# Performance work log

Hardware: AMD Instinct MI355X
Metric: run time of the kernel (lower is better)

Reference implementation:

```python
import jax, jax.numpy as jnp
import numpy as np

TEMPERATURE = 1.0
EPS = 1e-12


def _l2_normalize(x, axis):
    # torch F.normalize: x / max(||x||_2, eps)
    n = jnp.sqrt(jnp.sum(x * x, axis=axis, keepdims=True))
    return x / jnp.maximum(n, EPS)


def setup_inputs() -> dict:
    key = jax.random.key(0)
    k1, k2 = jax.random.split(key)
    B, C, H, W = 2, 128, 128, 256
    K = 20
    features = jax.random.normal(k1, (B, C, H, W), dtype=jnp.float32)
    prototypes = jax.random.normal(k2, (K, C), dtype=jnp.float32)
    distance_scale = jnp.ones((1,), dtype=jnp.float32)
    return {"features": features, "prototypes": prototypes, "distance_scale": distance_scale}


def reference(features, prototypes, distance_scale):
    # features: [B, C, H, W] -> transpose(1,3) -> [B, W, H, C]
    f = jnp.transpose(features, (0, 3, 2, 1))
    # torch F.normalize default dim=1: on [B, W, H, C] this is the W axis (faithful)
    fn = _l2_normalize(f, axis=1)
    # prototypes [K, C], normalized along dim=1 (features)
    pn = _l2_normalize(prototypes, axis=1)
    # exact euclidean cdist (donot_use_mm): broadcasted diff [B, W, H, K, C]
    diff = fn[:, :, :, None, :] - pn[None, None, None, :, :]
    dist = jnp.sqrt(jnp.sum(diff * diff, axis=-1))  # [B, W, H, K]
    dist = jnp.abs(distance_scale) * dist
    # transpose(3,1): [B, K, H, W]
    logits = -jnp.transpose(dist, (0, 3, 2, 1))
    return logits / TEMPERATURE
```

## Files before the change

kernel.cpp:

```cpp
#include <hip/hip_runtime.h>
#include <math.h>

#define B 2
#define C 128
#define H 128
#define W 256
#define K 20
#define HW (H * W)
#define SO_STRIDE 260

typedef float f32x4 __attribute__((ext_vector_type(4)));
typedef short bf16x8 __attribute__((ext_vector_type(8)));

__device__ __forceinline__ unsigned f2bf_bits(float x) {
    unsigned u = __float_as_uint(x);
    return (u + 0x7FFFu + ((u >> 16) & 1u)) >> 16;
}
__device__ __forceinline__ float bf_to_f(unsigned bits) {
    return __uint_as_float(bits << 16);
}

__global__ __launch_bounds__(1024) void isomax_fused(
    const float* __restrict__ feats, const float* __restrict__ protos,
    const float* __restrict__ dscale, float* __restrict__ out)
{
    __shared__ float s_rn[C];
    __shared__ float s_rp[32];
    __shared__ float s_pp[32];
    __shared__ float s_S[W];
    __shared__ __align__(16) float s_o[K * SO_STRIDE];

    const int tid  = threadIdx.x;
    const int wave = tid >> 6, lane = tid & 63;
    const int quad = lane >> 4, l16 = lane & 15;
    const int bh   = blockIdx.x;
    const int b    = bh >> 7, h = bh & 127;
    const int m0   = wave * 16;

    #pragma unroll
    for (int rd = 0; rd < 2; ++rd) {
        const int k = rd * 16 + wave;
        if (k < K) {
            const float* p = protos + k * C;
            const float a = p[lane], b2 = p[lane + 64];
            float ss = fmaf(a, a, b2 * b2);
            #pragma unroll
            for (int off = 32; off > 0; off >>= 1) ss += __shfl_xor(ss, off, 64);
            const float rp = 1.0f / fmaxf(sqrtf(ss), 1e-12f);
            const float q0 = bf_to_f(f2bf_bits(a * rp));
            const float q1 = bf_to_f(f2bf_bits(b2 * rp));
            float s2 = fmaf(q0, q0, q1 * q1);
            #pragma unroll
            for (int off = 32; off > 0; off >>= 1) s2 += __shfl_xor(s2, off, 64);
            if (lane == 0) { s_rp[k] = rp; s_pp[k] = s2; }
        }
    }

    for (int c = wave; c < C; c += 16) {
        const float* row = feats + ((size_t)((b * C + c) * H + h)) * W;
        const float4 v = ((const float4*)row)[lane];
        float ss = fmaf(v.x, v.x, fmaf(v.y, v.y, fmaf(v.z, v.z, v.w * v.w)));
        #pragma unroll
        for (int off = 32; off > 0; off >>= 1) ss += __shfl_xor(ss, off, 64);
        if (lane == 0) s_rn[c] = 1.0f / fmaxf(sqrtf(ss), 1e-12f);
    }
    __syncthreads();

    bf16x8 bfrag[4][2];
    #pragma unroll
    for (int t = 0; t < 2; ++t) {
        const int k = t * 16 + l16;
        const float rp = (k < K) ? s_rp[k] : 0.0f;
        #pragma unroll
        for (int ch = 0; ch < 4; ++ch) {
            bf16x8 f = {0, 0, 0, 0, 0, 0, 0, 0};
            if (k < K) {
                const float* pr = protos + k * C + ch * 32 + quad * 8;
                const float4 pa = *(const float4*)(pr);
                const float4 pb = *(const float4*)(pr + 4);
                f[0] = (short)f2bf_bits(pa.x * rp);
                f[1] = (short)f2bf_bits(pa.y * rp);
                f[2] = (short)f2bf_bits(pa.z * rp);
                f[3] = (short)f2bf_bits(pa.w * rp);
                f[4] = (short)f2bf_bits(pb.x * rp);
                f[5] = (short)f2bf_bits(pb.y * rp);
                f[6] = (short)f2bf_bits(pb.z * rp);
                f[7] = (short)f2bf_bits(pb.w * rp);
            }
            bfrag[ch][t] = f;
        }
    }

    f32x4 acc0 = {0.f, 0.f, 0.f, 0.f}, acc1 = {0.f, 0.f, 0.f, 0.f};
    float Sp = 0.f;
    const float* fbase = feats + ((size_t)(b * C) * H + h) * W + m0 + l16;
    #pragma unroll
    for (int ch = 0; ch < 4; ++ch) {
        bf16x8 af;
        #pragma unroll
        for (int j = 0; j < 8; ++j) {
            const int c = ch * 32 + quad * 8 + j;
            const float uf = fbase[(size_t)c * HW] * s_rn[c];
            const unsigned bits = f2bf_bits(uf);
            af[j] = (short)bits;
            const float ur = bf_to_f(bits);
            Sp = fmaf(ur, ur, Sp);
        }
        acc0 = __builtin_amdgcn_mfma_f32_16x16x32_bf16(af, bfrag[ch][0], acc0, 0, 0, 0);
        acc1 = __builtin_amdgcn_mfma_f32_16x16x32_bf16(af, bfrag[ch][1], acc1, 0, 0, 0);
    }

    Sp += __shfl_xor(Sp, 16, 64);
    Sp += __shfl_xor(Sp, 32, 64);
    if (lane < 16) s_S[m0 + lane] = Sp;
    __syncthreads();

    const float scale = fabsf(dscale[0]);
    const float pcol0 = s_pp[l16];
    const float pcol1 = (l16 < 4) ? s_pp[16 + l16] : 0.0f;
    #pragma unroll
    for (int r = 0; r < 4; ++r) {
        const int wl = m0 + quad * 4 + r;
        const float Sm = s_S[wl];
        const float d20 = fmaxf(Sm + pcol0 - 2.0f * acc0[r], 0.f);
        s_o[l16 * SO_STRIDE + wl] = -scale * sqrtf(d20);
        if (l16 < 4) {
            const float d21 = fmaxf(Sm + pcol1 - 2.0f * acc1[r], 0.f);
            s_o[(16 + l16) * SO_STRIDE + wl] = -scale * sqrtf(d21);
        }
    }
    __syncthreads();

    for (int i = tid; i < K * (W / 4); i += 1024) {
        const int k = i >> 6, g = i & 63;
        const float4 v = *(const float4*)&s_o[k * SO_STRIDE + g * 4];
        *(float4*)(out + ((size_t)(b * K + k)) * HW + h * W + g * 4) = v;
    }
}

extern "C" void kernel_launch(void* const* d_in, const int* in_sizes, int n_in,
                              void* d_out, int out_size, void* d_ws, size_t ws_size,
                              hipStream_t stream) {
    const float* feats  = (const float*)d_in[0];
    const float* protos = (const float*)d_in[1];
    const float* dscale = (const float*)d_in[2];
    float* out = (float*)d_out;

    isomax_fused<<<B * H, 1024, 0, stream>>>(feats, protos, dscale, out);
}
```

Before: 86.82 us.

## Stage normalized bf16 features in swizzled LDS instead of re-reading global

Each block now loads every feature row once with coalesced float4 loads, normalizes and packs it to bf16, and writes it into a 32 KB XOR-swizzled LDS tile, processing the channels in two passes. MFMA A-fragments are then read from LDS instead of through a second strided scalar pass over global memory. This removes the duplicate global read of the features and the uncoalesced per-channel loads. In exchange it adds extra barriers and a large LDS footprint that may limit blocks per CU.

```diff
diff --git a/kernel.cpp b/kernel.cpp
--- a/kernel.cpp
+++ b/kernel.cpp
@@ -24,7 +24,7 @@
     const float* __restrict__ feats, const float* __restrict__ protos,
     const float* __restrict__ dscale, float* __restrict__ out)
 {
-    __shared__ float s_rn[C];
+    __shared__ __align__(16) unsigned s_u32[64 * 128];
     __shared__ float s_rp[32];
     __shared__ float s_pp[32];
     __shared__ float s_S[W];
@@ -56,58 +56,74 @@
         }
     }
 
-    for (int c = wave; c < C; c += 16) {
-        const float* row = feats + ((size_t)((b * C + c) * H + h)) * W;
-        const float4 v = ((const float4*)row)[lane];
-        float ss = fmaf(v.x, v.x, fmaf(v.y, v.y, fmaf(v.z, v.z, v.w * v.w)));
-        #pragma unroll
-        for (int off = 32; off > 0; off >>= 1) ss += __shfl_xor(ss, off, 64);
-        if (lane == 0) s_rn[c] = 1.0f / fmaxf(sqrtf(ss), 1e-12f);
-    }
-    __syncthreads();
-
-    bf16x8 bfrag[4][2];
-    #pragma unroll
-    for (int t = 0; t < 2; ++t) {
-        const int k = t * 16 + l16;
-        const float rp = (k < K) ? s_rp[k] : 0.0f;
-        #pragma unroll
-        for (int ch = 0; ch < 4; ++ch) {
-            bf16x8 f = {0, 0, 0, 0, 0, 0, 0, 0};
-            if (k < K) {
-                const float* pr = protos + k * C + ch * 32 + quad * 8;
-                const float4 pa = *(const float4*)(pr);
-                const float4 pb = *(const float4*)(pr + 4);
-                f[0] = (short)f2bf_bits(pa.x * rp);
-                f[1] = (short)f2bf_bits(pa.y * rp);
-                f[2] = (short)f2bf_bits(pa.z * rp);
-                f[3] = (short)f2bf_bits(pa.w * rp);
-                f[4] = (short)f2bf_bits(pb.x * rp);
-                f[5] = (short)f2bf_bits(pb.y * rp);
-                f[6] = (short)f2bf_bits(pb.z * rp);
-                f[7] = (short)f2bf_bits(pb.w * rp);
-            }
-            bfrag[ch][t] = f;
-        }
-    }
-
     f32x4 acc0 = {0.f, 0.f, 0.f, 0.f}, acc1 = {0.f, 0.f, 0.f, 0.f};
     float Sp = 0.f;
-    const float* fbase = feats + ((size_t)(b * C) * H + h) * W + m0 + l16;
+    bf16x8 bfrag[4][2];
+
     #pragma unroll
-    for (int ch = 0; ch < 4; ++ch) {
-        bf16x8 af;
+    for (int pass = 0; pass < 2; ++pass) {
         #pragma unroll
-        for (int j = 0; j < 8; ++j) {
-            const int c = ch * 32 + quad * 8 + j;
-            const float uf = fbase[(size_t)c * HW] * s_rn[c];
-            const unsigned bits = f2bf_bits(uf);
-            af[j] = (short)bits;
-            const float ur = bf_to_f(bits);
-            Sp = fmaf(ur, ur, Sp);
+        for (int r = 0; r < 4; ++r) {
+            const int cc = wave * 4 + r;
+            const int c  = pass * 64 + cc;
+            const float* row = feats + ((size_t)((b * C + c) * H + h)) * W;
+            const float4 f4 = ((const float4*)row)[lane];
+            float ss = fmaf(f4.x, f4.x, fmaf(f4.y, f4.y, fmaf(f4.z, f4.z, f4.w * f4.w)));
+            #pragma unroll
+            for (int off = 32; off > 0; off >>= 1) ss += __shfl_xor(ss, off, 64);
+            const float rn = 1.0f / fmaxf(sqrtf(ss), 1e-12f);
+            const unsigned lo = f2bf_bits(f4.x * rn) | (f2bf_bits(f4.y * rn) << 16);
+            const unsigned hi = f2bf_bits(f4.z * rn) | (f2bf_bits(f4.w * rn) << 16);
+            const int word = cc * 128 + ((lane * 2) ^ (((cc >> 3) & 3) << 3));
+            uint2 pk; pk.x = lo; pk.y = hi;
+            *(uint2*)&s_u32[word] = pk;
         }
-        acc0 = __builtin_amdgcn_mfma_f32_16x16x32_bf16(af, bfrag[ch][0], acc0, 0, 0, 0);
-        acc1 = __builtin_amdgcn_mfma_f32_16x16x32_bf16(af, bfrag[ch][1], acc1, 0, 0, 0);
+        __syncthreads();
+
+        if (pass == 0) {
+            #pragma unroll
+            for (int t = 0; t < 2; ++t) {
+                const int k = t * 16 + l16;
+                const float rp = (k < K) ? s_rp[k] : 0.0f;
+                #pragma unroll
+                for (int ch = 0; ch < 4; ++ch) {
+                    bf16x8 f = {0, 0, 0, 0, 0, 0, 0, 0};
+                    if (k < K) {
+                        const float* pr = protos + k * C + ch * 32 + quad * 8;
+                        const float4 pa = *(const float4*)(pr);
+                        const float4 pb = *(const float4*)(pr + 4);
+                        f[0] = (short)f2bf_bits(pa.x * rp);
+                        f[1] = (short)f2bf_bits(pa.y * rp);
+                        f[2] = (short)f2bf_bits(pa.z * rp);
+                        f[3] = (short)f2bf_bits(pa.w * rp);
+                        f[4] = (short)f2bf_bits(pb.x * rp);
+                        f[5] = (short)f2bf_bits(pb.y * rp);
+                        f[6] = (short)f2bf_bits(pb.z * rp);
+                        f[7] = (short)f2bf_bits(pb.w * rp);
+                    }
+                    bfrag[ch][t] = f;
+                }
+            }
+        }
+
+        const int wadrw = ((m0 + l16) >> 1) ^ (quad << 3);
+        const unsigned sel = (unsigned)(l16 & 1);
+        #pragma unroll
+        for (int ch2 = 0; ch2 < 2; ++ch2) {
+            bf16x8 af;
+            #pragma unroll
+            for (int j = 0; j < 8; ++j) {
+                const int rowi = ch2 * 32 + quad * 8 + j;
+                const unsigned v = s_u32[rowi * 128 + wadrw];
+                af[j] = (short)(sel ? (v >> 16) : v);
+                const float ur = __uint_as_float(sel ? (v & 0xffff0000u) : (v << 16));
+                Sp = fmaf(ur, ur, Sp);
+            }
+            const int ch = pass * 2 + ch2;
+            acc0 = __builtin_amdgcn_mfma_f32_16x16x32_bf16(af, bfrag[ch][0], acc0, 0, 0, 0);
+            acc1 = __builtin_amdgcn_mfma_f32_16x16x32_bf16(af, bfrag[ch][1], acc1, 0, 0, 0);
+        }
+        __syncthreads();
     }
 
     Sp += __shfl_xor(Sp, 16, 64);
```

New measurement: 86.88 us. No clear change (+0.1%).

## Stage normalized bf16 feature tile in LDS to avoid re-reading global features

Applied to the files above, without the earlier changes.

Each block now loads its feature slice from global memory once into registers, computes the per-channel norms, and writes the normalized bf16-packed values into a swizzled shared-memory tile. The MFMA A-fragments are then read from LDS instead of issuing a second strided global read per element. Prototype normalization is also restructured so each wave handles two prototypes in parallel. This removes the duplicate global traffic and scattered loads at the cost of 64KB of extra LDS per block and more register pressure.

```diff
diff --git a/kernel.cpp b/kernel.cpp
--- a/kernel.cpp
+++ b/kernel.cpp
@@ -24,7 +24,7 @@
     const float* __restrict__ feats, const float* __restrict__ protos,
     const float* __restrict__ dscale, float* __restrict__ out)
 {
-    __shared__ float s_rn[C];
+    __shared__ __align__(16) unsigned s_u32[C * 128];
     __shared__ float s_rp[32];
     __shared__ float s_pp[32];
     __shared__ float s_S[W];
@@ -37,33 +37,80 @@
     const int b    = bh >> 7, h = bh & 127;
     const int m0   = wave * 16;
 
+    const float* fb = feats + (size_t)b * C * HW + h * W;
+
+    const int cA = wave * 8;
+    float4 fA[4];
     #pragma unroll
-    for (int rd = 0; rd < 2; ++rd) {
-        const int k = rd * 16 + wave;
-        if (k < K) {
-            const float* p = protos + k * C;
-            const float a = p[lane], b2 = p[lane + 64];
-            float ss = fmaf(a, a, b2 * b2);
-            #pragma unroll
-            for (int off = 32; off > 0; off >>= 1) ss += __shfl_xor(ss, off, 64);
-            const float rp = 1.0f / fmaxf(sqrtf(ss), 1e-12f);
-            const float q0 = bf_to_f(f2bf_bits(a * rp));
-            const float q1 = bf_to_f(f2bf_bits(b2 * rp));
-            float s2 = fmaf(q0, q0, q1 * q1);
-            #pragma unroll
-            for (int off = 32; off > 0; off >>= 1) s2 += __shfl_xor(s2, off, 64);
-            if (lane == 0) { s_rp[k] = rp; s_pp[k] = s2; }
+    for (int r = 0; r < 4; ++r)
+        fA[r] = ((const float4*)(fb + (size_t)(cA + r) * HW))[lane];
+
+    const int k0 = wave;
+    const int k1 = 16 + (wave & 3);
+    const float pa0 = protos[k0 * C + lane], pb0 = protos[k0 * C + lane + 64];
+    const float pa1 = protos[k1 * C + lane], pb1 = protos[k1 * C + lane + 64];
+
+    const int cB = cA + 4;
+    float4 fB[4];
+    #pragma unroll
+    for (int r = 0; r < 4; ++r)
+        fB[r] = ((const float4*)(fb + (size_t)(cB + r) * HW))[lane];
+
+    {
+        float ss0 = fmaf(pa0, pa0, pb0 * pb0);
+        float ss1 = fmaf(pa1, pa1, pb1 * pb1);
+        #pragma unroll
+        for (int off = 32; off > 0; off >>= 1) {
+            ss0 += __shfl_xor(ss0, off, 64);
+            ss1 += __shfl_xor(ss1, off, 64);
+        }
+        const float rp0 = 1.0f / fmaxf(sqrtf(ss0), 1e-12f);
+        const float rp1 = 1.0f / fmaxf(sqrtf(ss1), 1e-12f);
+        const float q00 = bf_to_f(f2bf_bits(pa0 * rp0));
+        const float q01 = bf_to_f(f2bf_bits(pb0 * rp0));
+        const float q10 = bf_to_f(f2bf_bits(pa1 * rp1));
+        const float q11 = bf_to_f(f2bf_bits(pb1 * rp1));
+        float s20 = fmaf(q00, q00, q01 * q01);
+        float s21 = fmaf(q10, q10, q11 * q11);
+        #pragma unroll
+        for (int off = 32; off > 0; off >>= 1) {
+            s20 += __shfl_xor(s20, off, 64);
+            s21 += __shfl_xor(s21, off, 64);
+        }
+        if (lane == 0) {
+            s_rp[k0] = rp0; s_pp[k0] = s20;
+            if (wave < 4) { s_rp[k1] = rp1; s_pp[k1] = s21; }
         }
     }
 
-    for (int c = wave; c < C; c += 16) {
-        const float* row = feats + ((size_t)((b * C + c) * H + h)) * W;
-        const float4 v = ((const float4*)row)[lane];
-        float ss = fmaf(v.x, v.x, fmaf(v.y, v.y, fmaf(v.z, v.z, v.w * v.w)));
-        #pragma unroll
-        for (int off = 32; off > 0; off >>= 1) ss += __shfl_xor(ss, off, 64);
-        if (lane == 0) s_rn[c] = 1.0f / fmaxf(sqrtf(ss), 1e-12f);
+    #define PROC_GROUP(fR, c0)                                                     \
+    {                                                                              \
+        float ss[4];                                                               \
+        _Pragma("unroll")                                                          \
+        for (int r = 0; r < 4; ++r) {                                              \
+            const float4 v = fR[r];                                                \
+            ss[r] = fmaf(v.x, v.x, fmaf(v.y, v.y, fmaf(v.z, v.z, v.w * v.w)));     \
+        }                                                                          \
+        _Pragma("unroll")                                                          \
+        for (int off = 32; off > 0; off >>= 1) {                                   \
+            _Pragma("unroll")                                                      \
+            for (int r = 0; r < 4; ++r) ss[r] += __shfl_xor(ss[r], off, 64);       \
+        }                                                                          \
+        _Pragma("unroll")                                                          \
+        for (int r = 0; r < 4; ++r) {                                              \
+            const float rn = 1.0f / fmaxf(sqrtf(ss[r]), 1e-12f);                   \
+            const float4 v = fR[r];                                                \
+            const unsigned lo = f2bf_bits(v.x * rn) | (f2bf_bits(v.y * rn) << 16); \
+            const unsigned hi = f2bf_bits(v.z * rn) | (f2bf_bits(v.w * rn) << 16); \
+            const int c = (c0) + r;                                                \
+            const int word = c * 128 + ((lane * 2) ^ (((c >> 3) & 3) << 3));       \
+            uint2 pk; pk.x = lo; pk.y = hi;                                        \
+            *(uint2*)&s_u32[word] = pk;                                            \
+        }                                                                          \
     }
+
+    PROC_GROUP(fA, cA)
+    PROC_GROUP(fB, cB)
     __syncthreads();
 
     bf16x8 bfrag[4][2];
@@ -93,17 +140,17 @@
 
     f32x4 acc0 = {0.f, 0.f, 0.f, 0.f}, acc1 = {0.f, 0.f, 0.f, 0.f};
     float Sp = 0.f;
-    const float* fbase = feats + ((size_t)(b * C) * H + h) * W + m0 + l16;
+    const int wadrw = ((m0 + l16) >> 1) ^ (quad << 3);
+    const unsigned sel = (unsigned)(l16 & 1);
     #pragma unroll
     for (int ch = 0; ch < 4; ++ch) {
         bf16x8 af;
         #pragma unroll
         for (int j = 0; j < 8; ++j) {
-            const int c = ch * 32 + quad * 8 + j;
-            const float uf = fbase[(size_t)c * HW] * s_rn[c];
-            const unsigned bits = f2bf_bits(uf);
-            af[j] = (short)bits;
-            const float ur = bf_to_f(bits);
+            const int rowi = ch * 32 + quad * 8 + j;
+            const unsigned v = s_u32[rowi * 128 + wadrw];
+            af[j] = (short)(sel ? (v >> 16) : v);
+            const float ur = __uint_as_float(sel ? (v & 0xffff0000u) : (v << 16));
             Sp = fmaf(ur, ur, Sp);
         }
         acc0 = __builtin_amdgcn_mfma_f32_16x16x32_bf16(af, bfrag[ch][0], acc0, 0, 0, 0);
```

Measured after the change: 86.63 us. About the same (-0.2%).
